# Optimization experiments

Measured on AMD Instinct MI355X. Metric: run time of the kernel, lower is better.

## Reference

```python
import jax, jax.numpy as jnp
import numpy as np

GATE_CAP = 15.0
NH = 8
DH = 128  # head_dim = embedding_dim // num_heads
EPS_BACKEND = 1e-6
EPS_NORM = 1e-6


def soft_cap(z, cap):
    return cap * jnp.tanh(z / cap)


def setup_inputs() -> dict:
    key = jax.random.key(0)
    ks = jax.random.split(key, 9)
    B, S, D = 2, 2048, 1024
    s = lambda n: (1.0 / np.sqrt(n)).astype(np.float32) if isinstance(n, np.ndarray) else np.float32(1.0 / np.sqrt(n))
    return {
        "x": jax.random.normal(ks[0], (B, S, D), jnp.float32),
        "Wq": jax.random.normal(ks[1], (D, D), jnp.float32) * s(D),
        "Wk": jax.random.normal(ks[2], (DH, D), jnp.float32) * s(D),
        "Wv": jax.random.normal(ks[3], (DH, D), jnp.float32) * s(D),
        "Wog": jax.random.normal(ks[4], (D, D), jnp.float32) * s(D),
        "Wi": jax.random.normal(ks[5], (NH, D), jnp.float32) * s(D),
        "bi": jnp.zeros((NH,), jnp.float32),
        "Wf": jax.random.normal(ks[6], (NH, D), jnp.float32) * s(D),
        "bf": jnp.ones((NH,), jnp.float32),
        "ln_w": jnp.ones((D,), jnp.float32),
        "Wout": jax.random.normal(ks[7], (D, D), jnp.float32) * s(D),
    }


def reference(x, Wq, Wk, Wv, Wog, Wi, bi, Wf, bf, ln_w, Wout):
    B, S, D = x.shape
    # projections (single weight mode, use_bias=False except gates)
    q = jnp.einsum("bsd,ed->bse", x, Wq).reshape(B, S, NH, DH).transpose(0, 2, 1, 3)  # [B,NH,S,DH]
    k = jnp.einsum("bsd,ed->bse", x, Wk)[:, None, :, :]  # [B,1,S,DH] (num_key_value_heads=1)
    v = jnp.einsum("bsd,ed->bse", x, Wv)[:, None, :, :]
    k = jnp.broadcast_to(k, (B, NH, S, DH))  # repeat_kv
    v = jnp.broadcast_to(v, (B, NH, S, DH))
    o_preact = jnp.einsum("bsd,ed->bse", x, Wog)  # [B,S,D]
    i_pre = soft_cap(jnp.einsum("bsd,hd->bhs", x, Wi) + bi[None, :, None], GATE_CAP)  # [B,NH,S]
    f_pre = soft_cap(jnp.einsum("bsd,hd->bhs", x, Wf) + bf[None, :, None], GATE_CAP)

    # native parallel mLSTM backend (stabilized), no initial state
    log_f = jax.nn.log_sigmoid(f_pre)               # [B,NH,S]
    csum = jnp.cumsum(log_f, axis=-1)
    mat_log_f = csum[:, :, :, None] - csum[:, :, None, :]  # [B,NH,S,S]
    ltr = jnp.tril(jnp.ones((S, S), dtype=bool))
    mat_log_f = jnp.where(ltr, mat_log_f, -jnp.inf)
    mat_log_d = mat_log_f + i_pre[:, :, None, :]
    vec_m = jnp.max(mat_log_d, axis=-1, keepdims=True)      # [B,NH,S,1]
    mat_d = jnp.exp(mat_log_d - vec_m)
    mat_s = jnp.einsum("bhsd,bhtd->bhst", q, k) * (DH ** -0.5)
    mat_c = mat_s * mat_d
    vec_n = jnp.maximum(jnp.abs(jnp.sum(mat_c, axis=-1, keepdims=True)), jnp.exp(-vec_m))
    C = mat_c / (vec_n + EPS_BACKEND)
    h = jnp.einsum("bhst,bhtd->bhsd", C, v)  # [B,NH,S,DH]

    # multihead layernorm (per-head, fp32 reductions, weight only)
    h = h.transpose(0, 2, 1, 3)  # [B,S,NH,DH]
    h32 = h.astype(jnp.float32)
    mu = jnp.mean(h32, axis=-1, keepdims=True)
    var = jnp.mean(jnp.square(h32 - mu), axis=-1, keepdims=True)
    h_norm = ((h32 - mu) * jax.lax.rsqrt(var + EPS_NORM)).astype(h.dtype)
    h_norm = h_norm * ln_w.reshape(NH, DH)[None, None, :, :]
    h_norm = h_norm.reshape(B, S, D)

    h_out = jax.nn.sigmoid(o_preact) * h_norm
    y = jnp.einsum("bsd,ed->bse", h_out, Wout)
    return y
```

## Files before the change

### kernel.cpp

```cpp
#include <hip/hip_runtime.h>


typedef __bf16 bf16x8 __attribute__((ext_vector_type(8)));
typedef float f32x4 __attribute__((ext_vector_type(4)));
typedef unsigned short us8 __attribute__((ext_vector_type(8)));
typedef unsigned short us4 __attribute__((ext_vector_type(4)));

__device__ __forceinline__ unsigned short f2bf(float f) {
    unsigned int u = __builtin_bit_cast(unsigned int, f);
    unsigned int r = u + 0x7fffu + ((u >> 16) & 1u);
    return (unsigned short)(r >> 16);
}
__device__ __forceinline__ float bf2f(unsigned short h) {
    unsigned int u = ((unsigned int)h) << 16;
    return __builtin_bit_cast(float, u);
}
__device__ __forceinline__ f32x4 mfma16(bf16x8 a, bf16x8 b, f32x4 c) {
    return __builtin_amdgcn_mfma_f32_16x16x32_bf16(a, b, c, 0, 0, 0);
}

__global__ __launch_bounds__(256) void k_split_bf16(const float* __restrict__ in,
                                                    unsigned short* __restrict__ hi,
                                                    unsigned short* __restrict__ lo, int n) {
    int i = blockIdx.x * 256 + threadIdx.x;
    if (i < n) {
        float f = in[i];
        unsigned short h = f2bf(f);
        hi[i] = h;
        lo[i] = f2bf(f - bf2f(h));
    }
}

__global__ __launch_bounds__(256) void build_wcat(const float* __restrict__ Wq,
                                                  const float* __restrict__ Wk,
                                                  const float* __restrict__ Wv,
                                                  const float* __restrict__ Wog,
                                                  unsigned short* __restrict__ wh,
                                                  unsigned short* __restrict__ wl) {
    int idx = blockIdx.x * 256 + threadIdx.x;
    if (idx >= 2304 * 1024) return;
    int row = idx >> 10, col = idx & 1023;
    float v;
    if (row < 1024)      v = Wq[(size_t)row * 1024 + col] * 0.08838834764831845f;
    else if (row < 1152) v = Wk[(size_t)(row - 1024) * 1024 + col];
    else if (row < 1280) v = Wv[(size_t)(row - 1152) * 1024 + col];
    else                 v = Wog[(size_t)(row - 1280) * 1024 + col];
    unsigned short h = f2bf(v);
    wh[idx] = h;
    wl[idx] = f2bf(v - bf2f(h));
}

__global__ __launch_bounds__(256) void gates_kernel(const float* __restrict__ x,
                                                    const float* __restrict__ Wi,
                                                    const float* __restrict__ bi,
                                                    const float* __restrict__ Wf,
                                                    const float* __restrict__ bfb,
                                                    float* __restrict__ ipre,
                                                    float* __restrict__ lgf) {
    int bs = blockIdx.x;
    int b = bs >> 11, s = bs & 2047;
    const float* xr = x + (size_t)bs * 1024;
    int lane = threadIdx.x & 63, w = threadIdx.x >> 6;
    const float* W = (w < 2) ? Wi : Wf;
    int h0 = (w & 1) * 4;
    float dot0 = 0.f, dot1 = 0.f, dot2 = 0.f, dot3 = 0.f;
    for (int i = lane; i < 1024; i += 64) {
        float xv = xr[i];
        dot0 += xv * W[(size_t)(h0 + 0) * 1024 + i];
        dot1 += xv * W[(size_t)(h0 + 1) * 1024 + i];
        dot2 += xv * W[(size_t)(h0 + 2) * 1024 + i];
        dot3 += xv * W[(size_t)(h0 + 3) * 1024 + i];
    }
#pragma unroll
    for (int o = 32; o; o >>= 1) {
        dot0 += __shfl_xor(dot0, o);
        dot1 += __shfl_xor(dot1, o);
        dot2 += __shfl_xor(dot2, o);
        dot3 += __shfl_xor(dot3, o);
    }
    if (lane == 0) {
        float d[4] = {dot0, dot1, dot2, dot3};
#pragma unroll
        for (int j = 0; j < 4; j++) {
            int hh = h0 + j;
            if (w < 2) {
                float z = d[j] + bi[hh];
                z = 15.f * tanhf(z * (1.f / 15.f));
                ipre[((size_t)b * 8 + hh) * 2048 + s] = z;
            } else {
                float z = d[j] + bfb[hh];
                z = 15.f * tanhf(z * (1.f / 15.f));
                lgf[((size_t)b * 8 + hh) * 2048 + s] = fminf(z, 0.f) - log1pf(expf(-fabsf(z)));
            }
        }
    }
}

__global__ void scan_kernel(const float* __restrict__ ipre, const float* __restrict__ lgf,
                            float* __restrict__ csum, float* __restrict__ aarr,
                            float* __restrict__ marr) {
    int bh = blockIdx.x;
    int lane = threadIdx.x;
    const float* lf = lgf + (size_t)bh * 2048;
    const float* ip = ipre + (size_t)bh * 2048;
    float* cs = csum + (size_t)bh * 2048;
    float* aa = aarr + (size_t)bh * 2048;
    float* mm = marr + (size_t)bh * 2048;
    float carry = 0.f;
    float carrym = -1e30f;
    for (int c = 0; c < 32; c++) {
        float v = lf[c * 64 + lane];
#pragma unroll
        for (int o = 1; o < 64; o <<= 1) {
            float t = __shfl_up(v, o);
            if (lane >= o) v += t;
        }
        float cval = carry + v;
        cs[c * 64 + lane] = cval;
        float a = ip[c * 64 + lane] - cval;
        aa[c * 64 + lane] = a;
        float mv = a;
#pragma unroll
        for (int o = 1; o < 64; o <<= 1) {
            float t = __shfl_up(mv, o);
            if (lane >= o) mv = fmaxf(mv, t);
        }
        float mval = fmaxf(carrym, mv);
        mm[c * 64 + lane] = mval;
        carry = __shfl(cval, 63);
        carrym = __shfl(mval, 63);
    }
}

__global__ __launch_bounds__(256) void gemm_bt3(const unsigned short* __restrict__ Ah,
                                                const unsigned short* __restrict__ Al,
                                                const unsigned short* __restrict__ Bh,
                                                const unsigned short* __restrict__ Bl,
                                                void* __restrict__ Cp,
                                                unsigned short* __restrict__ Clo,
                                                int K, int ldc, int c_bf16) {
    __shared__ __attribute__((aligned(16))) unsigned short Ash[128 * 40];
    __shared__ __attribute__((aligned(16))) unsigned short Asl[128 * 40];
    __shared__ __attribute__((aligned(16))) unsigned short Bsh[128 * 40];
    __shared__ __attribute__((aligned(16))) unsigned short Bsl[128 * 40];
    const int tid = threadIdx.x;
    const int lane = tid & 63, wv = tid >> 6;
    const int wr = wv >> 1, wc = wv & 1;
    const int fr = lane & 15, fg = lane >> 4;
    const int srow = tid >> 1, scol = (tid & 1) * 16;
    const size_t aoff = (size_t)(blockIdx.x * 128 + srow) * K + scol;
    const size_t boff = (size_t)(blockIdx.y * 128 + srow) * K + scol;
    f32x4 acc[4][4] = {};
    for (int kt = 0; kt < K; kt += 32) {
        us8 avh0 = *(const us8*)(Ah + aoff + kt);
        us8 avh1 = *(const us8*)(Ah + aoff + kt + 8);
        us8 avl0 = *(const us8*)(Al + aoff + kt);
        us8 avl1 = *(const us8*)(Al + aoff + kt + 8);
        us8 bvh0 = *(const us8*)(Bh + boff + kt);
        us8 bvh1 = *(const us8*)(Bh + boff + kt + 8);
        us8 bvl0 = *(const us8*)(Bl + boff + kt);
        us8 bvl1 = *(const us8*)(Bl + boff + kt + 8);
        __syncthreads();
        *(us8*)&Ash[srow * 40 + scol] = avh0;
        *(us8*)&Ash[srow * 40 + scol + 8] = avh1;
        *(us8*)&Asl[srow * 40 + scol] = avl0;
        *(us8*)&Asl[srow * 40 + scol + 8] = avl1;
        *(us8*)&Bsh[srow * 40 + scol] = bvh0;
        *(us8*)&Bsh[srow * 40 + scol + 8] = bvh1;
        *(us8*)&Bsl[srow * 40 + scol] = bvl0;
        *(us8*)&Bsl[srow * 40 + scol + 8] = bvl1;
        __syncthreads();
        bf16x8 bfh[4], bfl[4];
#pragma unroll
        for (int j = 0; j < 4; j++) {
            bfh[j] = __builtin_bit_cast(bf16x8, *(const us8*)&Bsh[(64 * wc + 16 * j + fr) * 40 + fg * 8]);
            bfl[j] = __builtin_bit_cast(bf16x8, *(const us8*)&Bsl[(64 * wc + 16 * j + fr) * 40 + fg * 8]);
        }
        __builtin_amdgcn_s_setprio(1);
#pragma unroll
        for (int i = 0; i < 4; i++) {
            bf16x8 afh = __builtin_bit_cast(bf16x8, *(const us8*)&Ash[(64 * wr + 16 * i + fr) * 40 + fg * 8]);
            bf16x8 afl = __builtin_bit_cast(bf16x8, *(const us8*)&Asl[(64 * wr + 16 * i + fr) * 40 + fg * 8]);
#pragma unroll
            for (int j = 0; j < 4; j++) {
                acc[i][j] = mfma16(afh, bfh[j], acc[i][j]);
                acc[i][j] = mfma16(afh, bfl[j], acc[i][j]);
                acc[i][j] = mfma16(afl, bfh[j], acc[i][j]);
            }
        }
        __builtin_amdgcn_s_setprio(0);
    }
#pragma unroll
    for (int i = 0; i < 4; i++)
#pragma unroll
        for (int j = 0; j < 4; j++)
#pragma unroll
            for (int e = 0; e < 4; e++) {
                int r = blockIdx.x * 128 + 64 * wr + 16 * i + fg * 4 + e;
                int c = blockIdx.y * 128 + 64 * wc + 16 * j + fr;
                float v = acc[i][j][e];
                if (c_bf16) {
                    unsigned short h = f2bf(v);
                    ((unsigned short*)Cp)[(size_t)r * ldc + c] = h;
                    Clo[(size_t)r * ldc + c] = f2bf(v - bf2f(h));
                } else {
                    ((float*)Cp)[(size_t)r * ldc + c] = v;
                }
            }
}

__global__ __launch_bounds__(256) void make_vt(const unsigned short* __restrict__ ph,
                                               const unsigned short* __restrict__ pl,
                                               unsigned short* __restrict__ vTh,
                                               unsigned short* __restrict__ vTl) {
    int i = blockIdx.x * 256 + threadIdx.x;
    if (i >= 524288) return;
    int s = i & 2047, c = (i >> 11) & 127, b = i >> 18;
    size_t src = ((size_t)(b * 2048 + s)) * 2304 + 1152 + c;
    vTh[i] = ph[src];
    vTl[i] = pl[src];
}

__global__ __launch_bounds__(256, 2) void attn_fused(const unsigned short* __restrict__ projh,
                                                     const unsigned short* __restrict__ projl,
                                                     const unsigned short* __restrict__ vTh,
                                                     const unsigned short* __restrict__ vTl,
                                                     const float* __restrict__ aarr,
                                                     const float* __restrict__ marr,
                                                     const float* __restrict__ csum,
                                                     const float* __restrict__ lnw,
                                                     unsigned short* __restrict__ ho_hi,
                                                     unsigned short* __restrict__ ho_lo) {
    __shared__ __attribute__((aligned(16))) unsigned short Klh[32 * 148];
    __shared__ __attribute__((aligned(16))) unsigned short Kll[32 * 148];
    __shared__ __attribute__((aligned(16))) unsigned short Vlh[128 * 40];
    __shared__ __attribute__((aligned(16))) unsigned short Vll[128 * 40];
    __shared__ float al[32];

    const int idx = blockIdx.x;
    const int half = idx >> 8;
    const int pid = idx & 255;
    const int bh = pid & 15;
    const int qt0 = pid >> 4;
    const int qt = half ? (31 - qt0) : qt0;
    const int b = bh >> 3, h = bh & 7;
    const int tid = threadIdx.x, lane = tid & 63, w = tid >> 6;
    const int fr = lane & 15, fg = lane >> 4;
    const int q0 = qt * 64;
    const int qg = q0 + 16 * w + fr;

    bf16x8 qfh[4], qfl[4];
    {
        const size_t qoff = (size_t)(b * 2048 + qg) * 2304 + h * 128;
#pragma unroll
        for (int ks = 0; ks < 4; ks++) {
            qfh[ks] = __builtin_bit_cast(bf16x8, *(const us8*)(projh + qoff + ks * 32 + fg * 8));
            qfl[ks] = __builtin_bit_cast(bf16x8, *(const us8*)(projl + qoff + ks * 32 + fg * 8));
        }
    }
    const float ma_q = marr[(size_t)bh * 2048 + qg];

    f32x4 acc[8] = {};
    float b_run = 0.f;

    const int kr = tid >> 3, kc = (tid & 7) * 16;
    const int vr = tid >> 1, vc = (tid & 1) * 16;
    const size_t kbase = (size_t)(b * 2048) * 2304 + 1024;
    const size_t vtbase = (size_t)b * 128 * 2048;

    const int nt = 2 * qt + 2;
    us8 kh0, kh1, kl0, kl1, vh0, vh1, vl0, vl1;
    float a_st;
#define LOADT(T0)                                                              \
    {                                                                          \
        const size_t ko = kbase + (size_t)((T0) + kr) * 2304 + kc;             \
        const size_t vo = vtbase + (size_t)vr * 2048 + (T0) + vc;              \
        kh0 = *(const us8*)(projh + ko);                                       \
        kh1 = *(const us8*)(projh + ko + 8);                                   \
        kl0 = *(const us8*)(projl + ko);                                       \
        kl1 = *(const us8*)(projl + ko + 8);                                   \
        vh0 = *(const us8*)(vTh + vo);                                         \
        vh1 = *(const us8*)(vTh + vo + 8);                                     \
        vl0 = *(const us8*)(vTl + vo);                                         \
        vl1 = *(const us8*)(vTl + vo + 8);                                     \
        a_st = (tid < 32) ? aarr[(size_t)bh * 2048 + (T0) + tid] : 0.f;        \
    }

    LOADT(0);
    for (int kt = 0; kt < nt; kt++) {
        const int t0 = kt * 32;
        __syncthreads();
        *(us8*)&Klh[kr * 148 + kc] = kh0;
        *(us8*)&Klh[kr * 148 + kc + 8] = kh1;
        *(us8*)&Kll[kr * 148 + kc] = kl0;
        *(us8*)&Kll[kr * 148 + kc + 8] = kl1;
        *(us8*)&Vlh[vr * 40 + vc] = vh0;
        *(us8*)&Vlh[vr * 40 + vc + 8] = vh1;
        *(us8*)&Vll[vr * 40 + vc] = vl0;
        *(us8*)&Vll[vr * 40 + vc + 8] = vl1;
        if (tid < 32) al[tid] = a_st;
        __syncthreads();
        if (kt + 1 < nt) LOADT(t0 + 32);

        float dj[2][4];
#pragma unroll
        for (int j = 0; j < 2; j++) {
            f32x4 sf = {};
            __builtin_amdgcn_s_setprio(1);
#pragma unroll
            for (int ks = 0; ks < 4; ks++) {
                bf16x8 kfh = __builtin_bit_cast(bf16x8, *(const us8*)&Klh[(j * 16 + fr) * 148 + ks * 32 + fg * 8]);
                bf16x8 kfl = __builtin_bit_cast(bf16x8, *(const us8*)&Kll[(j * 16 + fr) * 148 + ks * 32 + fg * 8]);
                sf = mfma16(kfh, qfh[ks], sf);
                sf = mfma16(kfh, qfl[ks], sf);
                sf = mfma16(kfl, qfh[ks], sf);
            }
            __builtin_amdgcn_s_setprio(0);
#pragma unroll
            for (int r = 0; r < 4; r++) {
                const int kloc = j * 16 + fg * 4 + r;
                const int key = t0 + kloc;
                const float atv = al[kloc];
                dj[j][r] = (key <= qg) ? sf[r] * __expf(atv - ma_q) : 0.f;
            }
        }

        {
            float ts = dj[0][0] + dj[0][1] + dj[0][2] + dj[0][3]
                     + dj[1][0] + dj[1][1] + dj[1][2] + dj[1][3];
            ts += __shfl_xor(ts, 16);
            ts += __shfl_xor(ts, 32);
            b_run += ts;
        }

        float p8[8];
        const int srlo = 32 * ((lane >> 4) & 1) + fr;
#pragma unroll
        for (int e = 0; e < 8; e++) {
            const int sl = srlo + ((e >= 4) ? 16 : 0);
            const float v0 = __shfl(dj[0][e & 3], sl);
            const float v1 = __shfl(dj[1][e & 3], sl);
            p8[e] = (lane & 32) ? v1 : v0;
        }
        us8 phu, plu;
#pragma unroll
        for (int e = 0; e < 8; e++) {
            unsigned short hh = f2bf(p8[e]);
            phu[e] = hh;
            plu[e] = f2bf(p8[e] - bf2f(hh));
        }
        const bf16x8 pfh = __builtin_bit_cast(bf16x8, phu);
        const bf16x8 pfl = __builtin_bit_cast(bf16x8, plu);

        __builtin_amdgcn_s_setprio(1);
#pragma unroll
        for (int jb = 0; jb < 8; jb++) {
            bf16x8 vfh = __builtin_bit_cast(bf16x8, *(const us8*)&Vlh[(jb * 16 + fr) * 40 + fg * 8]);
            bf16x8 vfl = __builtin_bit_cast(bf16x8, *(const us8*)&Vll[(jb * 16 + fr) * 40 + fg * 8]);
            acc[jb] = mfma16(vfh, pfh, acc[jb]);
            acc[jb] = mfma16(vfh, pfl, acc[jb]);
            acc[jb] = mfma16(vfl, pfh, acc[jb]);
        }
        __builtin_amdgcn_s_setprio(0);
    }
#undef LOADT

    const float cs_q = csum[(size_t)bh * 2048 + qg];
    const float nf = __expf(-(cs_q + ma_q));
    const float n = fmaxf(fabsf(b_run), nf);
    const float inv = 1.f / (n + 1e-6f);
#pragma unroll
    for (int jb = 0; jb < 8; jb++) acc[jb] *= inv;

    float s1 = 0.f;
#pragma unroll
    for (int jb = 0; jb < 8; jb++) s1 += acc[jb][0] + acc[jb][1] + acc[jb][2] + acc[jb][3];
    s1 += __shfl_xor(s1, 16);
    s1 += __shfl_xor(s1, 32);
    const float mu = s1 * (1.f / 128.f);
    float vv = 0.f;
#pragma unroll
    for (int jb = 0; jb < 8; jb++)
#pragma unroll
        for (int e = 0; e < 4; e++) {
            float d = acc[jb][e] - mu;
            vv += d * d;
        }
    vv += __shfl_xor(vv, 16);
    vv += __shfl_xor(vv, 32);
    const float rstd = rsqrtf(vv * (1.f / 128.f) + 1e-6f);

    const size_t obase = (size_t)(b * 2048 + qg) * 2304 + 1280 + h * 128 + fg * 4;
    const size_t hbase = (size_t)(b * 2048 + qg) * 1024 + h * 128 + fg * 4;
#pragma unroll
    for (int jb = 0; jb < 8; jb++) {
        us4 ogh = *(const us4*)(projh + obase + jb * 16);
        us4 ogl = *(const us4*)(projl + obase + jb * 16);
        f32x4 lw = *(const f32x4*)&lnw[h * 128 + jb * 16 + fg * 4];
        us4 hi4, lo4;
#pragma unroll
        for (int e = 0; e < 4; e++) {
            const float og = bf2f(ogh[e]) + bf2f(ogl[e]);
            const float sig = 1.f / (1.f + __expf(-og));
            const float ho = (acc[jb][e] - mu) * rstd * lw[e] * sig;
            unsigned short h1 = f2bf(ho);
            hi4[e] = h1;
            lo4[e] = f2bf(ho - bf2f(h1));
        }
        *(us4*)&ho_hi[hbase + jb * 16] = hi4;
        *(us4*)&ho_lo[hbase + jb * 16] = lo4;
    }
}

extern "C" void kernel_launch(void* const* d_in, const int* in_sizes, int n_in,
                              void* d_out, int out_size, void* d_ws, size_t ws_size,
                              hipStream_t stream) {
    (void)in_sizes; (void)n_in; (void)out_size; (void)ws_size;
    const float* x    = (const float*)d_in[0];
    const float* Wq   = (const float*)d_in[1];
    const float* Wk   = (const float*)d_in[2];
    const float* Wv   = (const float*)d_in[3];
    const float* Wog  = (const float*)d_in[4];
    const float* Wi   = (const float*)d_in[5];
    const float* bi   = (const float*)d_in[6];
    const float* Wf   = (const float*)d_in[7];
    const float* bfb  = (const float*)d_in[8];
    const float* lnw  = (const float*)d_in[9];
    const float* Wout = (const float*)d_in[10];

    char* p = (char*)d_ws;
    auto carve = [&](size_t bytes) -> char* {
        char* r = p;
        p += (bytes + 255) & ~(size_t)255;
        return r;
    };
    unsigned short* x_hi   = (unsigned short*)carve(4194304ull * 2);
    unsigned short* x_lo   = (unsigned short*)carve(4194304ull * 2);
    unsigned short* wc_hi  = (unsigned short*)carve(2359296ull * 2);
    unsigned short* wc_lo  = (unsigned short*)carve(2359296ull * 2);
    unsigned short* wo_hi  = (unsigned short*)carve(1048576ull * 2);
    unsigned short* wo_lo  = (unsigned short*)carve(1048576ull * 2);
    unsigned short* pr_hi  = (unsigned short*)carve(4096ull * 2304 * 2);
    unsigned short* pr_lo  = (unsigned short*)carve(4096ull * 2304 * 2);
    unsigned short* vT_hi  = (unsigned short*)carve(524288ull * 2);
    unsigned short* vT_lo  = (unsigned short*)carve(524288ull * 2);
    float* ipre    = (float*)carve(32768ull * 4);
    float* lgf_buf = (float*)carve(32768ull * 4);
    float* csum    = (float*)carve(32768ull * 4);
    float* aarr    = (float*)carve(32768ull * 4);
    float* marr    = (float*)carve(32768ull * 4);
    unsigned short* ho_hi = x_hi;
    unsigned short* ho_lo = x_lo;

    k_split_bf16<<<16384, 256, 0, stream>>>(x, x_hi, x_lo, 4194304);
    build_wcat<<<(2359296 + 255) / 256, 256, 0, stream>>>(Wq, Wk, Wv, Wog, wc_hi, wc_lo);
    k_split_bf16<<<4096, 256, 0, stream>>>(Wout, wo_hi, wo_lo, 1048576);
    gates_kernel<<<4096, 256, 0, stream>>>(x, Wi, bi, Wf, bfb, ipre, lgf_buf);
    scan_kernel<<<16, 64, 0, stream>>>(ipre, lgf_buf, csum, aarr, marr);
    gemm_bt3<<<dim3(32, 18), 256, 0, stream>>>(x_hi, x_lo, wc_hi, wc_lo, pr_hi, pr_lo, 1024, 2304, 1);
    make_vt<<<2048, 256, 0, stream>>>(pr_hi, pr_lo, vT_hi, vT_lo);
    attn_fused<<<512, 256, 0, stream>>>(pr_hi, pr_lo, vT_hi, vT_lo, aarr, marr, csum, lnw, ho_hi, ho_lo);
    gemm_bt3<<<dim3(32, 8), 256, 0, stream>>>(ho_hi, ho_lo, wo_hi, wo_lo, d_out, nullptr, 1024, 1024, 0);
}
```

Before: 326.9 us.

## Double-buffer K/V tiles in attention and tile the V transpose through LDS

The attention kernel now keeps two LDS buffers for the K/V/gate tiles. It writes the next tile into the alternate buffer while computing on the current one, which leaves one barrier per iteration instead of two. The score MFMAs are split into three independent accumulators to shorten the dependency chain. The V transpose kernel now stages 64x64 tiles through shared memory, so global reads and writes are vectorised and coalesced instead of scalar and strided. The cost is double the LDS per block, which may limit occupancy, and some extra registers for the accumulators.

```diff
diff --git a/kernel.cpp b/kernel.cpp
--- a/kernel.cpp
+++ b/kernel.cpp
@@ -213,12 +213,40 @@
                                                const unsigned short* __restrict__ pl,
                                                unsigned short* __restrict__ vTh,
                                                unsigned short* __restrict__ vTl) {
-    int i = blockIdx.x * 256 + threadIdx.x;
-    if (i >= 524288) return;
-    int s = i & 2047, c = (i >> 11) & 127, b = i >> 18;
-    size_t src = ((size_t)(b * 2048 + s)) * 2304 + 1152 + c;
-    vTh[i] = ph[src];
-    vTl[i] = pl[src];
+    __shared__ __attribute__((aligned(16))) unsigned short th[64 * 68];
+    __shared__ __attribute__((aligned(16))) unsigned short tl[64 * 68];
+    const int bid = blockIdx.x;
+    const int st = bid & 31, ct = (bid >> 5) & 1, b = bid >> 6;
+    const int tid = threadIdx.x;
+    {
+        const int sr = tid >> 2, cc = (tid & 3) * 16;
+        const size_t rbase = (size_t)(b * 2048 + st * 64 + sr) * 2304 + 1152 + ct * 64 + cc;
+        us8 a0 = *(const us8*)(ph + rbase);
+        us8 a1 = *(const us8*)(ph + rbase + 8);
+        us8 c0 = *(const us8*)(pl + rbase);
+        us8 c1 = *(const us8*)(pl + rbase + 8);
+        *(us8*)&th[sr * 68 + cc] = a0;
+        *(us8*)&th[sr * 68 + cc + 8] = a1;
+        *(us8*)&tl[sr * 68 + cc] = c0;
+        *(us8*)&tl[sr * 68 + cc + 8] = c1;
+    }
+    __syncthreads();
+    {
+        const int cr = tid >> 2, ss = (tid & 3) * 16;
+        us8 oh0, oh1, ol0, ol1;
+#pragma unroll
+        for (int e = 0; e < 8; e++) {
+            oh0[e] = th[(ss + e) * 68 + cr];
+            oh1[e] = th[(ss + 8 + e) * 68 + cr];
+            ol0[e] = tl[(ss + e) * 68 + cr];
+            ol1[e] = tl[(ss + 8 + e) * 68 + cr];
+        }
+        const size_t wbase = (size_t)b * 128 * 2048 + (size_t)(ct * 64 + cr) * 2048 + st * 64 + ss;
+        *(us8*)&vTh[wbase] = oh0;
+        *(us8*)&vTh[wbase + 8] = oh1;
+        *(us8*)&vTl[wbase] = ol0;
+        *(us8*)&vTl[wbase + 8] = ol1;
+    }
 }
 
 __global__ __launch_bounds__(256, 2) void attn_fused(const unsigned short* __restrict__ projh,
@@ -231,11 +259,11 @@
                                                      const float* __restrict__ lnw,
                                                      unsigned short* __restrict__ ho_hi,
                                                      unsigned short* __restrict__ ho_lo) {
-    __shared__ __attribute__((aligned(16))) unsigned short Klh[32 * 148];
-    __shared__ __attribute__((aligned(16))) unsigned short Kll[32 * 148];
-    __shared__ __attribute__((aligned(16))) unsigned short Vlh[128 * 40];
-    __shared__ __attribute__((aligned(16))) unsigned short Vll[128 * 40];
-    __shared__ float al[32];
+    __shared__ __attribute__((aligned(16))) unsigned short Klh[2][32 * 148];
+    __shared__ __attribute__((aligned(16))) unsigned short Kll[2][32 * 148];
+    __shared__ __attribute__((aligned(16))) unsigned short Vlh[2][128 * 40];
+    __shared__ __attribute__((aligned(16))) unsigned short Vll[2][128 * 40];
+    __shared__ float al[2][32];
 
     const int idx = blockIdx.x;
     const int half = idx >> 8;
@@ -285,42 +313,52 @@
         vl1 = *(const us8*)(vTl + vo + 8);                                     \
         a_st = (tid < 32) ? aarr[(size_t)bh * 2048 + (T0) + tid] : 0.f;        \
     }
+#define STORET(BUF)                                                            \
+    {                                                                          \
+        *(us8*)&Klh[BUF][kr * 148 + kc] = kh0;                                 \
+        *(us8*)&Klh[BUF][kr * 148 + kc + 8] = kh1;                             \
+        *(us8*)&Kll[BUF][kr * 148 + kc] = kl0;                                 \
+        *(us8*)&Kll[BUF][kr * 148 + kc + 8] = kl1;                             \
+        *(us8*)&Vlh[BUF][vr * 40 + vc] = vh0;                                  \
+        *(us8*)&Vlh[BUF][vr * 40 + vc + 8] = vh1;                              \
+        *(us8*)&Vll[BUF][vr * 40 + vc] = vl0;                                  \
+        *(us8*)&Vll[BUF][vr * 40 + vc + 8] = vl1;                              \
+        if (tid < 32) al[BUF][tid] = a_st;                                     \
+    }
 
     LOADT(0);
+    STORET(0);
+    if (nt > 1) LOADT(32);
+    __syncthreads();
+
     for (int kt = 0; kt < nt; kt++) {
+        const int cur = kt & 1;
         const int t0 = kt * 32;
-        __syncthreads();
-        *(us8*)&Klh[kr * 148 + kc] = kh0;
-        *(us8*)&Klh[kr * 148 + kc + 8] = kh1;
-        *(us8*)&Kll[kr * 148 + kc] = kl0;
-        *(us8*)&Kll[kr * 148 + kc + 8] = kl1;
-        *(us8*)&Vlh[vr * 40 + vc] = vh0;
-        *(us8*)&Vlh[vr * 40 + vc + 8] = vh1;
-        *(us8*)&Vll[vr * 40 + vc] = vl0;
-        *(us8*)&Vll[vr * 40 + vc + 8] = vl1;
-        if (tid < 32) al[tid] = a_st;
-        __syncthreads();
-        if (kt + 1 < nt) LOADT(t0 + 32);
+        if (kt + 1 < nt) {
+            STORET(cur ^ 1);
+            if (kt + 2 < nt) LOADT((kt + 2) * 32);
+        }
 
         float dj[2][4];
 #pragma unroll
         for (int j = 0; j < 2; j++) {
-            f32x4 sf = {};
+            f32x4 sfa = {}, sfb = {}, sfc = {};
             __builtin_amdgcn_s_setprio(1);
 #pragma unroll
             for (int ks = 0; ks < 4; ks++) {
-                bf16x8 kfh = __builtin_bit_cast(bf16x8, *(const us8*)&Klh[(j * 16 + fr) * 148 + ks * 32 + fg * 8]);
-                bf16x8 kfl = __builtin_bit_cast(bf16x8, *(const us8*)&Kll[(j * 16 + fr) * 148 + ks * 32 + fg * 8]);
-                sf = mfma16(kfh, qfh[ks], sf);
-                sf = mfma16(kfh, qfl[ks], sf);
-                sf = mfma16(kfl, qfh[ks], sf);
+                bf16x8 kfh = __builtin_bit_cast(bf16x8, *(const us8*)&Klh[cur][(j * 16 + fr) * 148 + ks * 32 + fg * 8]);
+                bf16x8 kfl = __builtin_bit_cast(bf16x8, *(const us8*)&Kll[cur][(j * 16 + fr) * 148 + ks * 32 + fg * 8]);
+                sfa = mfma16(kfh, qfh[ks], sfa);
+                sfb = mfma16(kfh, qfl[ks], sfb);
+                sfc = mfma16(kfl, qfh[ks], sfc);
             }
             __builtin_amdgcn_s_setprio(0);
+            f32x4 sf = (sfa + sfb) + sfc;
 #pragma unroll
             for (int r = 0; r < 4; r++) {
                 const int kloc = j * 16 + fg * 4 + r;
                 const int key = t0 + kloc;
-                const float atv = al[kloc];
+                const float atv = al[cur][kloc];
                 dj[j][r] = (key <= qg) ? sf[r] * __expf(atv - ma_q) : 0.f;
             }
         }
@@ -355,15 +393,17 @@
         __builtin_amdgcn_s_setprio(1);
 #pragma unroll
         for (int jb = 0; jb < 8; jb++) {
-            bf16x8 vfh = __builtin_bit_cast(bf16x8, *(const us8*)&Vlh[(jb * 16 + fr) * 40 + fg * 8]);
-            bf16x8 vfl = __builtin_bit_cast(bf16x8, *(const us8*)&Vll[(jb * 16 + fr) * 40 + fg * 8]);
+            bf16x8 vfh = __builtin_bit_cast(bf16x8, *(const us8*)&Vlh[cur][(jb * 16 + fr) * 40 + fg * 8]);
+            bf16x8 vfl = __builtin_bit_cast(bf16x8, *(const us8*)&Vll[cur][(jb * 16 + fr) * 40 + fg * 8]);
             acc[jb] = mfma16(vfh, pfh, acc[jb]);
             acc[jb] = mfma16(vfh, pfl, acc[jb]);
             acc[jb] = mfma16(vfl, pfh, acc[jb]);
         }
         __builtin_amdgcn_s_setprio(0);
+        __syncthreads();
     }
 #undef LOADT
+#undef STORET
 
     const float cs_q = csum[(size_t)bh * 2048 + qg];
     const float nf = __expf(-(cs_q + ma_q));
@@ -458,7 +498,7 @@
     gates_kernel<<<4096, 256, 0, stream>>>(x, Wi, bi, Wf, bfb, ipre, lgf_buf);
     scan_kernel<<<16, 64, 0, stream>>>(ipre, lgf_buf, csum, aarr, marr);
     gemm_bt3<<<dim3(32, 18), 256, 0, stream>>>(x_hi, x_lo, wc_hi, wc_lo, pr_hi, pr_lo, 1024, 2304, 1);
-    make_vt<<<2048, 256, 0, stream>>>(pr_hi, pr_lo, vT_hi, vT_lo);
+    make_vt<<<128, 256, 0, stream>>>(pr_hi, pr_lo, vT_hi, vT_lo);
     attn_fused<<<512, 256, 0, stream>>>(pr_hi, pr_lo, vT_hi, vT_lo, aarr, marr, csum, lnw, ho_hi, ho_lo);
     gemm_bt3<<<dim3(32, 8), 256, 0, stream>>>(ho_hi, ho_lo, wo_hi, wo_lo, d_out, nullptr, 1024, 1024, 0);
 }
```

New measurement: 319.5 us. 2.3% less time.

## Split attention key range across two blocks and combine in separate kernel

Applied to the files above, without the earlier changes.

The fused attention kernel is split into a partial kernel that processes either the first or second half of each query tile's key tiles, writing unnormalized fp32 partial outputs and row sums to workspace. A new combine kernel then adds the partials and applies normalization, layernorm, sigmoid gating and the bf16 hi/lo split. The grid doubles to 1024 blocks with higher occupancy bounds to fill more CUs, at the cost of extra global traffic for the partials and one more launch. The V-transpose kernel is also rewritten to use an LDS tile for coalesced reads and writes, and the three MFMA chains now go to separate accumulators to shorten dependency chains.

```diff
diff --git a/kernel.cpp b/kernel.cpp
--- a/kernel.cpp
+++ b/kernel.cpp
@@ -3,8 +3,10 @@
 
 typedef __bf16 bf16x8 __attribute__((ext_vector_type(8)));
 typedef float f32x4 __attribute__((ext_vector_type(4)));
+typedef float f32x2 __attribute__((ext_vector_type(2)));
 typedef unsigned short us8 __attribute__((ext_vector_type(8)));
 typedef unsigned short us4 __attribute__((ext_vector_type(4)));
+typedef unsigned short us2 __attribute__((ext_vector_type(2)));
 
 __device__ __forceinline__ unsigned short f2bf(float f) {
     unsigned int u = __builtin_bit_cast(unsigned int, f);
@@ -213,24 +215,50 @@
                                                const unsigned short* __restrict__ pl,
                                                unsigned short* __restrict__ vTh,
                                                unsigned short* __restrict__ vTl) {
-    int i = blockIdx.x * 256 + threadIdx.x;
-    if (i >= 524288) return;
-    int s = i & 2047, c = (i >> 11) & 127, b = i >> 18;
-    size_t src = ((size_t)(b * 2048 + s)) * 2304 + 1152 + c;
-    vTh[i] = ph[src];
-    vTl[i] = pl[src];
-}
-
-__global__ __launch_bounds__(256, 2) void attn_fused(const unsigned short* __restrict__ projh,
-                                                     const unsigned short* __restrict__ projl,
-                                                     const unsigned short* __restrict__ vTh,
-                                                     const unsigned short* __restrict__ vTl,
-                                                     const float* __restrict__ aarr,
-                                                     const float* __restrict__ marr,
-                                                     const float* __restrict__ csum,
-                                                     const float* __restrict__ lnw,
-                                                     unsigned short* __restrict__ ho_hi,
-                                                     unsigned short* __restrict__ ho_lo) {
+    __shared__ __attribute__((aligned(16))) unsigned short th[64 * 68];
+    __shared__ __attribute__((aligned(16))) unsigned short tl[64 * 68];
+    const int bid = blockIdx.x;
+    const int st = bid & 31, ct = (bid >> 5) & 1, b = bid >> 6;
+    const int tid = threadIdx.x;
+    {
+        const int sr = tid >> 2, cc = (tid & 3) * 16;
+        const size_t rbase = (size_t)(b * 2048 + st * 64 + sr) * 2304 + 1152 + ct * 64 + cc;
+        us8 a0 = *(const us8*)(ph + rbase);
+        us8 a1 = *(const us8*)(ph + rbase + 8);
+        us8 c0 = *(const us8*)(pl + rbase);
+        us8 c1 = *(const us8*)(pl + rbase + 8);
+        *(us8*)&th[sr * 68 + cc] = a0;
+        *(us8*)&th[sr * 68 + cc + 8] = a1;
+        *(us8*)&tl[sr * 68 + cc] = c0;
+        *(us8*)&tl[sr * 68 + cc + 8] = c1;
+    }
+    __syncthreads();
+    {
+        const int cr = tid >> 2, ss = (tid & 3) * 16;
+        us8 oh0, oh1, ol0, ol1;
+#pragma unroll
+        for (int e = 0; e < 8; e++) {
+            oh0[e] = th[(ss + e) * 68 + cr];
+            oh1[e] = th[(ss + 8 + e) * 68 + cr];
+            ol0[e] = tl[(ss + e) * 68 + cr];
+            ol1[e] = tl[(ss + 8 + e) * 68 + cr];
+        }
+        const size_t wbase = (size_t)b * 128 * 2048 + (size_t)(ct * 64 + cr) * 2048 + st * 64 + ss;
+        *(us8*)&vTh[wbase] = oh0;
+        *(us8*)&vTh[wbase + 8] = oh1;
+        *(us8*)&vTl[wbase] = ol0;
+        *(us8*)&vTl[wbase + 8] = ol1;
+    }
+}
+
+__global__ __launch_bounds__(256, 4) void attn_part(const unsigned short* __restrict__ projh,
+                                                    const unsigned short* __restrict__ projl,
+                                                    const unsigned short* __restrict__ vTh,
+                                                    const unsigned short* __restrict__ vTl,
+                                                    const float* __restrict__ aarr,
+                                                    const float* __restrict__ marr,
+                                                    float* __restrict__ Opart,
+                                                    float* __restrict__ bpart) {
     __shared__ __attribute__((aligned(16))) unsigned short Klh[32 * 148];
     __shared__ __attribute__((aligned(16))) unsigned short Kll[32 * 148];
     __shared__ __attribute__((aligned(16))) unsigned short Vlh[128 * 40];
@@ -238,8 +266,10 @@
     __shared__ float al[32];
 
     const int idx = blockIdx.x;
-    const int half = idx >> 8;
-    const int pid = idx & 255;
+    const int piece = idx >> 9;
+    const int sub = idx & 511;
+    const int half = sub >> 8;
+    const int pid = sub & 255;
     const int bh = pid & 15;
     const int qt0 = pid >> 4;
     const int qt = half ? (31 - qt0) : qt0;
@@ -249,6 +279,11 @@
     const int q0 = qt * 64;
     const int qg = q0 + 16 * w + fr;
 
+    const int nt = 2 * qt + 2;
+    const int mid = qt + 1;
+    const int t_begin = piece ? mid : 0;
+    const int t_end = piece ? nt : mid;
+
     bf16x8 qfh[4], qfl[4];
     {
         const size_t qoff = (size_t)(b * 2048 + qg) * 2304 + h * 128;
@@ -268,7 +303,6 @@
     const size_t kbase = (size_t)(b * 2048) * 2304 + 1024;
     const size_t vtbase = (size_t)b * 128 * 2048;
 
-    const int nt = 2 * qt + 2;
     us8 kh0, kh1, kl0, kl1, vh0, vh1, vl0, vl1;
     float a_st;
 #define LOADT(T0)                                                              \
@@ -286,8 +320,8 @@
         a_st = (tid < 32) ? aarr[(size_t)bh * 2048 + (T0) + tid] : 0.f;        \
     }
 
-    LOADT(0);
-    for (int kt = 0; kt < nt; kt++) {
+    LOADT(t_begin * 32);
+    for (int kt = t_begin; kt < t_end; kt++) {
         const int t0 = kt * 32;
         __syncthreads();
         *(us8*)&Klh[kr * 148 + kc] = kh0;
@@ -300,22 +334,23 @@
         *(us8*)&Vll[vr * 40 + vc + 8] = vl1;
         if (tid < 32) al[tid] = a_st;
         __syncthreads();
-        if (kt + 1 < nt) LOADT(t0 + 32);
+        if (kt + 1 < t_end) LOADT(t0 + 32);
 
         float dj[2][4];
 #pragma unroll
         for (int j = 0; j < 2; j++) {
-            f32x4 sf = {};
+            f32x4 sfa = {}, sfb = {}, sfc = {};
             __builtin_amdgcn_s_setprio(1);
 #pragma unroll
             for (int ks = 0; ks < 4; ks++) {
                 bf16x8 kfh = __builtin_bit_cast(bf16x8, *(const us8*)&Klh[(j * 16 + fr) * 148 + ks * 32 + fg * 8]);
                 bf16x8 kfl = __builtin_bit_cast(bf16x8, *(const us8*)&Kll[(j * 16 + fr) * 148 + ks * 32 + fg * 8]);
-                sf = mfma16(kfh, qfh[ks], sf);
-                sf = mfma16(kfh, qfl[ks], sf);
-                sf = mfma16(kfl, qfh[ks], sf);
+                sfa = mfma16(kfh, qfh[ks], sfa);
+                sfb = mfma16(kfh, qfl[ks], sfb);
+                sfc = mfma16(kfl, qfh[ks], sfc);
             }
             __builtin_amdgcn_s_setprio(0);
+            f32x4 sf = (sfa + sfb) + sfc;
 #pragma unroll
             for (int r = 0; r < 4; r++) {
                 const int kloc = j * 16 + fg * 4 + r;
@@ -365,51 +400,71 @@
     }
 #undef LOADT
 
-    const float cs_q = csum[(size_t)bh * 2048 + qg];
-    const float nf = __expf(-(cs_q + ma_q));
-    const float n = fmaxf(fabsf(b_run), nf);
+    const size_t prow = ((size_t)piece * 32768 + bh * 2048 + qg) * 128;
+#pragma unroll
+    for (int jb = 0; jb < 8; jb++)
+        *(f32x4*)&Opart[prow + jb * 16 + fg * 4] = acc[jb];
+    if (fg == 0)
+        bpart[(size_t)piece * 32768 + bh * 2048 + qg] = b_run;
+}
+
+__global__ __launch_bounds__(256) void combine(const float* __restrict__ Opart,
+                                               const float* __restrict__ bpart,
+                                               const float* __restrict__ csum,
+                                               const float* __restrict__ marr,
+                                               const unsigned short* __restrict__ projh,
+                                               const unsigned short* __restrict__ projl,
+                                               const float* __restrict__ lnw,
+                                               unsigned short* __restrict__ ho_hi,
+                                               unsigned short* __restrict__ ho_lo) {
+    const int row = blockIdx.x * 4 + (threadIdx.x >> 6);
+    const int lane = threadIdx.x & 63;
+    const int bh = row >> 11, s = row & 2047;
+    const int b = bh >> 3, h = bh & 7;
+
+    const float b_tot = bpart[row] + bpart[32768 + row];
+    const float cs = csum[row];
+    const float ma = marr[row];
+    const float nf = __expf(-(cs + ma));
+    const float n = fmaxf(fabsf(b_tot), nf);
     const float inv = 1.f / (n + 1e-6f);
-#pragma unroll
-    for (int jb = 0; jb < 8; jb++) acc[jb] *= inv;
-
-    float s1 = 0.f;
-#pragma unroll
-    for (int jb = 0; jb < 8; jb++) s1 += acc[jb][0] + acc[jb][1] + acc[jb][2] + acc[jb][3];
-    s1 += __shfl_xor(s1, 16);
-    s1 += __shfl_xor(s1, 32);
+
+    const int ch = lane * 2;
+    f32x2 oa = *(const f32x2*)&Opart[(size_t)row * 128 + ch];
+    f32x2 ob = *(const f32x2*)&Opart[((size_t)32768 + row) * 128 + ch];
+    const float v0 = (oa[0] + ob[0]) * inv;
+    const float v1 = (oa[1] + ob[1]) * inv;
+
+    float s1 = v0 + v1;
+#pragma unroll
+    for (int o = 1; o < 64; o <<= 1) s1 += __shfl_xor(s1, o);
     const float mu = s1 * (1.f / 128.f);
-    float vv = 0.f;
-#pragma unroll
-    for (int jb = 0; jb < 8; jb++)
-#pragma unroll
-        for (int e = 0; e < 4; e++) {
-            float d = acc[jb][e] - mu;
-            vv += d * d;
-        }
-    vv += __shfl_xor(vv, 16);
-    vv += __shfl_xor(vv, 32);
+    float vv = (v0 - mu) * (v0 - mu) + (v1 - mu) * (v1 - mu);
+#pragma unroll
+    for (int o = 1; o < 64; o <<= 1) vv += __shfl_xor(vv, o);
     const float rstd = rsqrtf(vv * (1.f / 128.f) + 1e-6f);
 
-    const size_t obase = (size_t)(b * 2048 + qg) * 2304 + 1280 + h * 128 + fg * 4;
-    const size_t hbase = (size_t)(b * 2048 + qg) * 1024 + h * 128 + fg * 4;
-#pragma unroll
-    for (int jb = 0; jb < 8; jb++) {
-        us4 ogh = *(const us4*)(projh + obase + jb * 16);
-        us4 ogl = *(const us4*)(projl + obase + jb * 16);
-        f32x4 lw = *(const f32x4*)&lnw[h * 128 + jb * 16 + fg * 4];
-        us4 hi4, lo4;
-#pragma unroll
-        for (int e = 0; e < 4; e++) {
-            const float og = bf2f(ogh[e]) + bf2f(ogl[e]);
-            const float sig = 1.f / (1.f + __expf(-og));
-            const float ho = (acc[jb][e] - mu) * rstd * lw[e] * sig;
-            unsigned short h1 = f2bf(ho);
-            hi4[e] = h1;
-            lo4[e] = f2bf(ho - bf2f(h1));
-        }
-        *(us4*)&ho_hi[hbase + jb * 16] = hi4;
-        *(us4*)&ho_lo[hbase + jb * 16] = lo4;
-    }
+    const size_t ogo = (size_t)(b * 2048 + s) * 2304 + 1280 + h * 128 + ch;
+    us2 ogh = *(const us2*)&projh[ogo];
+    us2 ogl = *(const us2*)&projl[ogo];
+    const float og0 = bf2f(ogh[0]) + bf2f(ogl[0]);
+    const float og1 = bf2f(ogh[1]) + bf2f(ogl[1]);
+    const float sig0 = 1.f / (1.f + __expf(-og0));
+    const float sig1 = 1.f / (1.f + __expf(-og1));
+
+    f32x2 lw = *(const f32x2*)&lnw[h * 128 + ch];
+    const float ho0 = (v0 - mu) * rstd * lw[0] * sig0;
+    const float ho1 = (v1 - mu) * rstd * lw[1] * sig1;
+
+    const size_t hoff = (size_t)(b * 2048 + s) * 1024 + h * 128 + ch;
+    us2 oh, ol;
+    unsigned short h0b = f2bf(ho0);
+    unsigned short h1b = f2bf(ho1);
+    oh[0] = h0b; oh[1] = h1b;
+    ol[0] = f2bf(ho0 - bf2f(h0b));
+    ol[1] = f2bf(ho1 - bf2f(h1b));
+    *(us2*)&ho_hi[hoff] = oh;
+    *(us2*)&ho_lo[hoff] = ol;
 }
 
 extern "C" void kernel_launch(void* const* d_in, const int* in_sizes, int n_in,
@@ -449,6 +504,8 @@
     float* csum    = (float*)carve(32768ull * 4);
     float* aarr    = (float*)carve(32768ull * 4);
     float* marr    = (float*)carve(32768ull * 4);
+    float* Opart   = (float*)carve(2ull * 32768 * 128 * 4);
+    float* bpart   = (float*)carve(2ull * 32768 * 4);
     unsigned short* ho_hi = x_hi;
     unsigned short* ho_lo = x_lo;
 
@@ -458,7 +515,8 @@
     gates_kernel<<<4096, 256, 0, stream>>>(x, Wi, bi, Wf, bfb, ipre, lgf_buf);
     scan_kernel<<<16, 64, 0, stream>>>(ipre, lgf_buf, csum, aarr, marr);
     gemm_bt3<<<dim3(32, 18), 256, 0, stream>>>(x_hi, x_lo, wc_hi, wc_lo, pr_hi, pr_lo, 1024, 2304, 1);
-    make_vt<<<2048, 256, 0, stream>>>(pr_hi, pr_lo, vT_hi, vT_lo);
-    attn_fused<<<512, 256, 0, stream>>>(pr_hi, pr_lo, vT_hi, vT_lo, aarr, marr, csum, lnw, ho_hi, ho_lo);
+    make_vt<<<128, 256, 0, stream>>>(pr_hi, pr_lo, vT_hi, vT_lo);
+    attn_part<<<1024, 256, 0, stream>>>(pr_hi, pr_lo, vT_hi, vT_lo, aarr, marr, Opart, bpart);
+    combine<<<8192, 256, 0, stream>>>(Opart, bpart, csum, marr, pr_hi, pr_lo, lnw, ho_hi, ho_lo);
     gemm_bt3<<<dim3(32, 8), 256, 0, stream>>>(ho_hi, ho_lo, wo_hi, wo_lo, d_out, nullptr, 1024, 1024, 0);
 }
```

Result: slower. 410.5 us (+25.6%).
